# Kernel tuning notes

Hardware: AMD Instinct MI355X
Metric: run time of the kernel (lower is better)

Reference implementation:

```python
import jax, jax.numpy as jnp
import numpy as np

N_NODES = 100000
N_EDGES = 3200000
NFEAT, NHID, NCLASS = 512, 128, 40


def _glorot(key, fan_in, fan_out):
    lim = jnp.sqrt(6.0 / (fan_in + fan_out))
    return jax.random.uniform(key, (fan_in, fan_out), jnp.float32, -lim, lim)


def setup_inputs() -> dict:
    key = jax.random.key(0)
    k1, k2, k3, k4, k5 = jax.random.split(key, 5)
    x = jax.random.normal(k1, (N_NODES, NFEAT), jnp.float32)
    edge_index = jax.random.randint(k2, (2, N_EDGES), 0, N_NODES, jnp.int64)
    edge_weight = jax.random.uniform(k3, (N_EDGES,), jnp.float32)
    W1 = _glorot(k4, NFEAT, NHID)
    b1 = jnp.zeros((NHID,), jnp.float32)
    W2 = _glorot(k5, NHID, NCLASS)
    b2 = jnp.zeros((NCLASS,), jnp.float32)
    return {"x": x, "edge_index": edge_index, "edge_weight": edge_weight,
            "W1": W1, "b1": b1, "W2": W2, "b2": b2}


def _gcn_norm(edge_index, edge_weight, num_nodes):
    # add self loops (weight 1), symmetric normalization D^-1/2 A D^-1/2
    loop = jnp.arange(num_nodes, dtype=edge_index.dtype)
    row = jnp.concatenate([edge_index[0], loop])
    col = jnp.concatenate([edge_index[1], loop])
    w = jnp.concatenate([edge_weight, jnp.ones((num_nodes,), edge_weight.dtype)])
    deg = jax.ops.segment_sum(w, col, num_segments=num_nodes)
    dinv = jnp.where(deg > 0, jax.lax.rsqrt(jnp.maximum(deg, 1e-20)), 0.0)
    norm = dinv[row] * w * dinv[col]
    return row, col, norm


def _gcn_conv(h, row, col, norm, W, b, num_nodes):
    h = h @ W                                  # [N, out]
    msg = norm[:, None] * h[row]               # per-edge gather + scale
    out = jax.ops.segment_sum(msg, col, num_segments=num_nodes)  # scatter-add
    return out + b


def reference(x, edge_index, edge_weight, W1, b1, W2, b2):
    n = x.shape[0]
    row, col, norm = _gcn_norm(edge_index, edge_weight, n)
    h = jax.nn.relu(_gcn_conv(x, row, col, norm, W1, b1, n))
    # dropout: eval mode (training=False) -> identity
    return _gcn_conv(h, row, col, norm, W2, b2, n)
```

## Files before the change

kernel.cpp:

```cpp
#include <hip/hip_runtime.h>

#define NN 100000
#define NE 3200000
#define NF 512
#define NH 128
#define NC 40
#define NBIN 196
#define BINW 512
#define CAP  20480
#define EPB  4096

typedef __attribute__((ext_vector_type(8))) short bfrag;
typedef __attribute__((ext_vector_type(4))) float f32x4;
typedef __attribute__((ext_vector_type(8))) unsigned short u16x8;

static __device__ __forceinline__ unsigned short f2bf(float x) {
  unsigned u = __float_as_uint(x);
  u += 0x7FFF + ((u >> 16) & 1);
  return (unsigned short)(u >> 16);
}
static __device__ __forceinline__ float bf2f(unsigned short b) {
  return __uint_as_float(((unsigned)b) << 16);
}
static __device__ __forceinline__ float bflo(unsigned u) { return __uint_as_float(u << 16); }
static __device__ __forceinline__ float bfhi(unsigned u) { return __uint_as_float(u & 0xFFFF0000u); }


__global__ __launch_bounds__(256) void k_wconv(const float* __restrict__ W1,
                                               unsigned short* __restrict__ Wfh,
                                               unsigned short* __restrict__ Wfl,
                                               int* __restrict__ binfill) {
  if (blockIdx.x == 0 && threadIdx.x < NBIN) binfill[threadIdx.x] = 0;
  int i = blockIdx.x * 256 + threadIdx.x;
  int k = i >> 7, n = i & 127;
  float w = W1[i];
  unsigned short hi = f2bf(w);
  unsigned short lo = f2bf(w - bf2f(hi));
  int idx = ((k >> 3) * 128 + n) * 8 + (k & 7);
  Wfh[idx] = hi; Wfl[idx] = lo;
}


__global__ __launch_bounds__(256) void k_binA(const int* __restrict__ row, const int* __restrict__ col,
                                              const float* __restrict__ w,
                                              int* __restrict__ binfill, int2* __restrict__ binned) {
  __shared__ int hist[NBIN];
  __shared__ int base[NBIN];
  int t = threadIdx.x;
  int eb = blockIdx.x * EPB;
  for (int i = t; i < NBIN; i += 256) hist[i] = 0;
  __syncthreads();
  int rk[16], bn[16], sr[16]; float wv[16];
#pragma unroll
  for (int j = 0; j < 16; ++j) {
    int e = eb + t + j * 256;
    if (e < NE) {
      int c = __builtin_nontemporal_load(col + e);
      bn[j] = c >> 9;
      sr[j] = __builtin_nontemporal_load(row + e) | ((c & 511) << 17);
      wv[j] = __builtin_nontemporal_load(w + e);
      rk[j] = atomicAdd(&hist[bn[j]], 1);
    } else bn[j] = -1;
  }
  __syncthreads();
  if (t < NBIN) { int hv = hist[t]; base[t] = hv ? atomicAdd(&binfill[t], hv) : 0; }
  __syncthreads();
#pragma unroll
  for (int j = 0; j < 16; ++j) {
    if (bn[j] >= 0) {
      int pos = base[bn[j]] + rk[j];
      if (pos < CAP) binned[(size_t)bn[j] * CAP + pos] = make_int2(sr[j], __float_as_int(wv[j]));
    }
  }
}


__global__ __launch_bounds__(256) void k_binscan(const int* __restrict__ binfill,
                                                 int* __restrict__ binptr, int* __restrict__ rowptr) {
  __shared__ int sm[256];
  int t = threadIdx.x;
  sm[t] = (t < NBIN) ? binfill[t] : 0;
  __syncthreads();
  for (int off = 1; off < 256; off <<= 1) {
    int a = (t >= off) ? sm[t - off] : 0;
    __syncthreads();
    sm[t] += a;
    __syncthreads();
  }
  if (t <= NBIN) binptr[t] = (t == 0) ? 0 : sm[t - 1];
  if (t == 0) rowptr[NN] = NE;
}


__global__ __launch_bounds__(256) void k_binB(const int* __restrict__ binfill, const int* __restrict__ binptr,
                                              const int2* __restrict__ binned, int2* __restrict__ pair,
                                              int* __restrict__ rowptr, float* __restrict__ dinv) {
  __shared__ unsigned long long pk[BINW];
  __shared__ unsigned short lrank[CAP];
  __shared__ int lptr[BINW];
  __shared__ int sm[256];
  int t = threadIdx.x;
  int bin = blockIdx.x;
  int cnt = binfill[bin]; if (cnt > CAP) cnt = CAP;
  int bb = binptr[bin];
  pk[t] = 0ULL; pk[t + 256] = 0ULL;
  __syncthreads();
  const int2* src = binned + (size_t)bin * CAP;
  for (int i = t; i < cnt; i += 256) {
    int2 r = src[i];
    int lc = (unsigned)r.x >> 17;
    unsigned long long fw = (unsigned long long)(unsigned)(__int_as_float(r.y) * 16777216.0f + 0.5f);
    unsigned long long old = atomicAdd(&pk[lc], (1ULL << 42) | fw);
    lrank[i] = (unsigned short)(old >> 42);
  }
  __syncthreads();
  int c0 = (int)(pk[2 * t] >> 42), c1 = (int)(pk[2 * t + 1] >> 42);
  sm[t] = c0 + c1;
  __syncthreads();
  for (int off = 1; off < 256; off <<= 1) {
    int a = (t >= off) ? sm[t - off] : 0;
    __syncthreads();
    sm[t] += a;
    __syncthreads();
  }
  int excl = (t == 0) ? 0 : sm[t - 1];
  lptr[2 * t] = excl;
  lptr[2 * t + 1] = excl + c0;
  int n0 = bin * BINW + 2 * t;
  if (n0 < NN) {
    rowptr[n0] = bb + excl;
    float d = (float)(pk[2 * t] & 0x3FFFFFFFFFFULL) * (1.0f / 16777216.0f) + 1.0f;
    dinv[n0] = rsqrtf(d);
  }
  if (n0 + 1 < NN) {
    rowptr[n0 + 1] = bb + excl + c0;
    float d = (float)(pk[2 * t + 1] & 0x3FFFFFFFFFFULL) * (1.0f / 16777216.0f) + 1.0f;
    dinv[n0 + 1] = rsqrtf(d);
  }
  __syncthreads();
  for (int i = t; i < cnt; i += 256) {
    int2 r = src[i];
    int lc = (unsigned)r.x >> 17;
    int pos = bb + lptr[lc] + (int)lrank[i];
    pair[pos] = make_int2(r.x & 0x1FFFF, r.y);
  }
}


__global__ __launch_bounds__(256) void k_gemm1(const float* __restrict__ X,
                                               const unsigned short* __restrict__ Wfh,
                                               const unsigned short* __restrict__ Wfl,
                                               const float* __restrict__ dinv,
                                               unsigned short* __restrict__ HXb) {
  __shared__ unsigned short Ah[4096], Bh[4096], Bl[4096];
  int t = threadIdx.x;
  int lane = t & 63;
  int wid = t >> 6;
  int m0 = blockIdx.x * 128;
  int sm = t & 127;
  int skh = t >> 7;
  const float* xrow = X + (size_t)(m0 + sm) * NF + skh * 16;
  bool mok = (m0 + sm) < NN;
  int wm = wid >> 1, wn = wid & 1;
  int mb = wm * 64, nb = wn * 64;
  int fr = lane & 15, fg = lane >> 4;

  f32x4 acc[4][4];
#pragma unroll
  for (int i = 0; i < 4; ++i)
#pragma unroll
    for (int j = 0; j < 4; ++j) acc[i][j] = (f32x4)0.0f;

  for (int ks = 0; ks < 16; ++ks) {
    const u16x8* sh = (const u16x8*)(Wfh + (size_t)ks * 4096);
    const u16x8* sl = (const u16x8*)(Wfl + (size_t)ks * 4096);
    u16x8 b0 = sh[t], b1 = sh[t + 256];
    u16x8 c0 = sl[t], c1 = sl[t + 256];
    float4 xv[4];
#pragma unroll
    for (int q = 0; q < 4; ++q) {
      xv[q] = mok ? *(const float4*)(xrow + ks * 32 + q * 4)
                  : make_float4(0.f, 0.f, 0.f, 0.f);
    }
#pragma unroll
    for (int q = 0; q < 4; ++q) {
      float f[4] = {xv[q].x, xv[q].y, xv[q].z, xv[q].w};
      unsigned short h[4];
#pragma unroll
      for (int j = 0; j < 4; ++j) h[j] = f2bf(f[j]);
      int lk = skh * 16 + q * 4;
      int base = ((lk >> 3) * 128 + sm) * 8 + (lk & 7);
      uint2 hv = make_uint2((unsigned)h[0] | ((unsigned)h[1] << 16),
                            (unsigned)h[2] | ((unsigned)h[3] << 16));
      *(uint2*)&Ah[base] = hv;
    }
    ((u16x8*)Bh)[t] = b0; ((u16x8*)Bh)[t + 256] = b1;
    ((u16x8*)Bl)[t] = c0; ((u16x8*)Bl)[t + 256] = c1;
    __syncthreads();
    bfrag ah[4], bh[4], bl[4];
#pragma unroll
    for (int mi = 0; mi < 4; ++mi)
      ah[mi] = *(bfrag*)&Ah[(fg * 128 + mb + mi * 16 + fr) * 8];
#pragma unroll
    for (int nt = 0; nt < 4; ++nt) {
      int idx = (fg * 128 + nb + nt * 16 + fr) * 8;
      bh[nt] = *(bfrag*)&Bh[idx];
      bl[nt] = *(bfrag*)&Bl[idx];
    }
#pragma unroll
    for (int mi = 0; mi < 4; ++mi)
#pragma unroll
      for (int nt = 0; nt < 4; ++nt) {
        acc[mi][nt] = __builtin_amdgcn_mfma_f32_16x16x32_bf16(ah[mi], bh[nt], acc[mi][nt], 0, 0, 0);
        acc[mi][nt] = __builtin_amdgcn_mfma_f32_16x16x32_bf16(ah[mi], bl[nt], acc[mi][nt], 0, 0, 0);
      }
    __syncthreads();
  }
#pragma unroll
  for (int mi = 0; mi < 4; ++mi) {
    int rb = m0 + mb + mi * 16 + fg * 4;
#pragma unroll
    for (int q = 0; q < 4; ++q) {
      int r = rb + q;
      if (r < NN) {
        float dv = dinv[r];
#pragma unroll
        for (int nt = 0; nt < 4; ++nt) {
          int c = nb + nt * 16 + fr;
          __builtin_nontemporal_store(f2bf(dv * acc[mi][nt][q]), HXb + (size_t)r * NH + c);
        }
      }
    }
  }
}


#define FMA8(n, v)                                            \
  { unsigned uu[4] = {(v).x, (v).y, (v).z, (v).w};            \
    _Pragma("unroll")                                         \
    for (int q = 0; q < 4; ++q) {                             \
      ax[q] = fmaf((n), bflo(uu[q]), ax[q]);                  \
      ay[q] = fmaf((n), bfhi(uu[q]), ay[q]);                  \
    } }

__global__ __launch_bounds__(256) void k_agg1(const int* __restrict__ rowptr, const int2* __restrict__ pair,
                                              const unsigned* __restrict__ hxb, const float* __restrict__ dinv,
                                              const float* __restrict__ b1, unsigned* __restrict__ hb) {
  int wid = (blockIdx.x * 256 + threadIdx.x) >> 6;
  int lane = threadIdx.x & 63;
  if (wid >= NN) return;
  int sub = lane >> 4, fl = lane & 15;
  int beg = rowptr[wid], end = rowptr[wid + 1];
  const uint4* hx4 = (const uint4*)hxb;
  const long long* pr = (const long long*)pair;
  float ax[4] = {0.f, 0.f, 0.f, 0.f}, ay[4] = {0.f, 0.f, 0.f, 0.f};
  int e = beg;
  for (; e + 16 <= end; e += 16) {
    long long r0 = pr[e + sub];
    long long r1 = pr[e + 4 + sub];
    long long r2 = pr[e + 8 + sub];
    long long r3 = pr[e + 12 + sub];
    uint4 v0 = hx4[(size_t)(unsigned)(r0 & 0x1FFFF) * 16 + fl];
    uint4 v1 = hx4[(size_t)(unsigned)(r1 & 0x1FFFF) * 16 + fl];
    uint4 v2 = hx4[(size_t)(unsigned)(r2 & 0x1FFFF) * 16 + fl];
    uint4 v3 = hx4[(size_t)(unsigned)(r3 & 0x1FFFF) * 16 + fl];
    float n0 = __int_as_float((int)(r0 >> 32));
    float n1 = __int_as_float((int)(r1 >> 32));
    float n2 = __int_as_float((int)(r2 >> 32));
    float n3 = __int_as_float((int)(r3 >> 32));
    FMA8(n0, v0);
    FMA8(n1, v1);
    FMA8(n2, v2);
    FMA8(n3, v3);
  }
  for (; e + 8 <= end; e += 8) {
    long long r0 = pr[e + sub];
    long long r1 = pr[e + 4 + sub];
    uint4 v0 = hx4[(size_t)(unsigned)(r0 & 0x1FFFF) * 16 + fl];
    uint4 v1 = hx4[(size_t)(unsigned)(r1 & 0x1FFFF) * 16 + fl];
    float n0 = __int_as_float((int)(r0 >> 32));
    float n1 = __int_as_float((int)(r1 >> 32));
    FMA8(n0, v0);
    FMA8(n1, v1);
  }
  for (; e < end; e += 4) {
    int idx = e + sub;
    bool ok = idx < end;
    long long r0 = ok ? pr[idx] : 0;
    unsigned s = ok ? (unsigned)(r0 & 0x1FFFF) : (unsigned)wid;
    float n0 = ok ? __int_as_float((int)(r0 >> 32)) : 0.f;
    uint4 v0 = hx4[(size_t)s * 16 + fl];
    FMA8(n0, v0);
  }
  if (sub == 0) {
    uint4 ov = hx4[(size_t)wid * 16 + fl];
    FMA8(1.0f, ov);
  }
#pragma unroll
  for (int q = 0; q < 4; ++q) {
    ax[q] += __shfl_xor(ax[q], 16, 64); ay[q] += __shfl_xor(ay[q], 16, 64);
    ax[q] += __shfl_xor(ax[q], 32, 64); ay[q] += __shfl_xor(ay[q], 32, 64);
  }
  if (sub == 0) {
    float di = dinv[wid];
    float4 bA = ((const float4*)b1)[fl * 2];
    float4 bB = ((const float4*)b1)[fl * 2 + 1];
    float bxs[4] = {bA.x, bA.z, bB.x, bB.z};
    float bys[4] = {bA.y, bA.w, bB.y, bB.w};
    unsigned o[4];
#pragma unroll
    for (int q = 0; q < 4; ++q) {
      float rx = fmaxf(fmaf(di, ax[q], bxs[q]), 0.f);
      float ry = fmaxf(fmaf(di, ay[q], bys[q]), 0.f);
      o[q] = (unsigned)f2bf(rx) | ((unsigned)f2bf(ry) << 16);
    }
    ((uint4*)hb)[(size_t)wid * 16 + fl] = make_uint4(o[0], o[1], o[2], o[3]);
  }
}


__global__ __launch_bounds__(256) void k_gemm2(const unsigned* __restrict__ hb, const float* __restrict__ W2,
                                               const float* __restrict__ dinv,
                                               unsigned short* __restrict__ H2b) {
  __shared__ float Hs[32][132];
  __shared__ float Ws[NH * NC];
  int t = threadIdx.x;
  int m0 = blockIdx.x * 32;
  {
    int r = t >> 3, cb = (t & 7) * 8;
    int rowi = m0 + r;
    if (rowi < NN) {
      uint4 a = *(const uint4*)(hb + (size_t)rowi * 64 + cb);
      uint4 b = *(const uint4*)(hb + (size_t)rowi * 64 + cb + 4);
      unsigned u[8] = {a.x, a.y, a.z, a.w, b.x, b.y, b.z, b.w};
#pragma unroll
      for (int j = 0; j < 8; ++j) {
        Hs[r][cb * 2 + j * 2]     = bflo(u[j]);
        Hs[r][cb * 2 + j * 2 + 1] = bfhi(u[j]);
      }
    } else {
#pragma unroll
      for (int j = 0; j < 16; ++j) Hs[r][cb * 2 + j] = 0.f;
    }
  }
  for (int i = t; i < NH * NC; i += 256) Ws[i] = W2[i];
  __syncthreads();
  int r = t >> 3, c0 = (t & 7) * 5;
  float acc[5] = {0.f, 0.f, 0.f, 0.f, 0.f};
#pragma unroll 4
  for (int k = 0; k < NH; ++k) {
    float hv = Hs[r][k];
#pragma unroll
    for (int j = 0; j < 5; ++j) acc[j] = fmaf(hv, Ws[k * NC + c0 + j], acc[j]);
  }
  int rowi = m0 + r;
  if (rowi < NN) {
    float dv = dinv[rowi];
#pragma unroll
    for (int j = 0; j < 5; ++j)
      __builtin_nontemporal_store(f2bf(dv * acc[j]), H2b + (size_t)rowi * 64 + c0 + j);
    int prr = t & 7;
    if (prr < 3) {
#pragma unroll
      for (int j = 0; j < 8; ++j)
        __builtin_nontemporal_store((unsigned short)0, H2b + (size_t)rowi * 64 + 40 + prr * 8 + j);
    }
  }
}


#define FMA4(n, v)                                            \
  { unsigned uu[2] = {(v).x, (v).y};                          \
    _Pragma("unroll")                                         \
    for (int q = 0; q < 2; ++q) {                             \
      ax[q] = fmaf((n), bflo(uu[q]), ax[q]);                  \
      ay[q] = fmaf((n), bfhi(uu[q]), ay[q]);                  \
    } }

__global__ __launch_bounds__(256) void k_agg2(const int* __restrict__ rowptr, const int2* __restrict__ pair,
                                              const unsigned* __restrict__ h2u,
                                              const float* __restrict__ dinv,
                                              const float* __restrict__ b2, float* __restrict__ out) {
  int wid = (blockIdx.x * 256 + threadIdx.x) >> 6;
  int lane = threadIdx.x & 63;
  if (wid >= NN) return;
  int sub = lane >> 4, fl = lane & 15;
  int beg = rowptr[wid], end = rowptr[wid + 1];
  const uint2* h4 = (const uint2*)h2u;
  const long long* pr = (const long long*)pair;
  float ax[2] = {0.f, 0.f}, ay[2] = {0.f, 0.f};
  int e = beg;
  for (; e + 16 <= end; e += 16) {
    long long r0 = pr[e + sub];
    long long r1 = pr[e + 4 + sub];
    long long r2 = pr[e + 8 + sub];
    long long r3 = pr[e + 12 + sub];
    uint2 v0 = h4[(size_t)(unsigned)(r0 & 0x1FFFF) * 16 + fl];
    uint2 v1 = h4[(size_t)(unsigned)(r1 & 0x1FFFF) * 16 + fl];
    uint2 v2 = h4[(size_t)(unsigned)(r2 & 0x1FFFF) * 16 + fl];
    uint2 v3 = h4[(size_t)(unsigned)(r3 & 0x1FFFF) * 16 + fl];
    float n0 = __int_as_float((int)(r0 >> 32));
    float n1 = __int_as_float((int)(r1 >> 32));
    float n2 = __int_as_float((int)(r2 >> 32));
    float n3 = __int_as_float((int)(r3 >> 32));
    FMA4(n0, v0);
    FMA4(n1, v1);
    FMA4(n2, v2);
    FMA4(n3, v3);
  }
  for (; e + 8 <= end; e += 8) {
    long long r0 = pr[e + sub];
    long long r1 = pr[e + 4 + sub];
    uint2 v0 = h4[(size_t)(unsigned)(r0 & 0x1FFFF) * 16 + fl];
    uint2 v1 = h4[(size_t)(unsigned)(r1 & 0x1FFFF) * 16 + fl];
    float n0 = __int_as_float((int)(r0 >> 32));
    float n1 = __int_as_float((int)(r1 >> 32));
    FMA4(n0, v0);
    FMA4(n1, v1);
  }
  for (; e < end; e += 4) {
    int idx = e + sub;
    bool ok = idx < end;
    long long r0 = ok ? pr[idx] : 0;
    unsigned s = ok ? (unsigned)(r0 & 0x1FFFF) : (unsigned)wid;
    float n0 = ok ? __int_as_float((int)(r0 >> 32)) : 0.f;
    uint2 v0 = h4[(size_t)s * 16 + fl];
    FMA4(n0, v0);
  }
  if (sub == 0) {
    uint2 ov = h4[(size_t)wid * 16 + fl];
    FMA4(1.0f, ov);
  }
#pragma unroll
  for (int q = 0; q < 2; ++q) {
    ax[q] += __shfl_xor(ax[q], 16, 64); ay[q] += __shfl_xor(ay[q], 16, 64);
    ax[q] += __shfl_xor(ax[q], 32, 64); ay[q] += __shfl_xor(ay[q], 32, 64);
  }
  if (sub == 0 && fl < 10) {
    float di = dinv[wid];
    float4 bv = ((const float4*)b2)[fl];
    float4 o = make_float4(fmaf(di, ax[0], bv.x), fmaf(di, ay[0], bv.y),
                           fmaf(di, ax[1], bv.z), fmaf(di, ay[1], bv.w));
    *(float4*)(out + (size_t)wid * NC + fl * 4) = o;
  }
}


extern "C" void kernel_launch(void* const* d_in, const int* in_sizes, int n_in,
                              void* d_out, int out_size, void* d_ws, size_t ws_size,
                              hipStream_t stream) {
  const float* x  = (const float*)d_in[0];
  const int*   ei = (const int*)d_in[1];
  const float* ew = (const float*)d_in[2];
  const float* W1 = (const float*)d_in[3];
  const float* b1 = (const float*)d_in[4];
  const float* W2 = (const float*)d_in[5];
  const float* b2 = (const float*)d_in[6];
  float* out = (float*)d_out;
  const int* row = ei;
  const int* col = ei + NE;

  char* ws = (char*)d_ws;
  size_t o = 0;
  auto alloc = [&](size_t bytes) -> void* {
    void* p = ws + o;
    o += (bytes + 255) & ~(size_t)255;
    return p;
  };
  float* dinv    = (float*)alloc((size_t)NN * 4);
  int*   rowptr  = (int*)alloc((size_t)(NN + 1) * 4);
  int*   binfill = (int*)alloc(1024);
  int*   binptr  = (int*)alloc(1024);
  int2*  pair    = (int2*)alloc((size_t)NE * 8);
  unsigned short* Wfh = (unsigned short*)alloc((size_t)NF * NH * 2);
  unsigned short* Wfl = (unsigned short*)alloc((size_t)NF * NH * 2);
  unsigned short* hxb = (unsigned short*)alloc((size_t)NN * NH * 2);
  unsigned*       hb  = (unsigned*)alloc((size_t)NN * NH * 2);
  int2*  binned  = (int2*)alloc((size_t)NBIN * CAP * 8);
  unsigned short* h2b = (unsigned short*)hxb;

  k_wconv<<<(NF * NH) / 256, 256, 0, stream>>>(W1, Wfh, Wfl, binfill);
  k_binA<<<(NE + EPB - 1) / EPB, 256, 0, stream>>>(row, col, ew, binfill, binned);
  k_binscan<<<1, 256, 0, stream>>>(binfill, binptr, rowptr);
  k_binB<<<NBIN, 256, 0, stream>>>(binfill, binptr, binned, pair, rowptr, dinv);
  k_gemm1<<<(NN + 127) / 128, 256, 0, stream>>>(x, Wfh, Wfl, dinv, hxb);
  k_agg1<<<(NN * 64) / 256, 256, 0, stream>>>(rowptr, pair, (const unsigned*)hxb, dinv, b1, hb);
  k_gemm2<<<(NN + 31) / 32, 256, 0, stream>>>(hb, W2, dinv, h2b);
  k_agg2<<<(NN * 64) / 256, 256, 0, stream>>>(rowptr, pair, (const unsigned*)h2b, dinv, b2, out);
}
```

Baseline: 400.8 us.

## Double-buffer LDS and prefetch next K-slice in first GEMM

```diff
diff --git a/kernel.cpp b/kernel.cpp
--- a/kernel.cpp
+++ b/kernel.cpp
@@ -152,7 +152,7 @@
                                                const unsigned short* __restrict__ Wfl,
                                                const float* __restrict__ dinv,
                                                unsigned short* __restrict__ HXb) {
-  __shared__ unsigned short Ah[4096], Bh[4096], Bl[4096];
+  __shared__ unsigned short Ah[2][4096], Bh[2][4096], Bl[2][4096];
   int t = threadIdx.x;
   int lane = t & 63;
   int wid = t >> 6;
@@ -171,17 +171,20 @@
 #pragma unroll
     for (int j = 0; j < 4; ++j) acc[i][j] = (f32x4)0.0f;
 
+  u16x8 vb0, vb1, vc0, vc1;
+  float4 xv[4];
+  {
+    const u16x8* sh = (const u16x8*)Wfh;
+    const u16x8* sl = (const u16x8*)Wfl;
+    vb0 = sh[t]; vb1 = sh[t + 256];
+    vc0 = sl[t]; vc1 = sl[t + 256];
+#pragma unroll
+    for (int q = 0; q < 4; ++q)
+      xv[q] = mok ? *(const float4*)(xrow + q * 4) : make_float4(0.f, 0.f, 0.f, 0.f);
+  }
+
   for (int ks = 0; ks < 16; ++ks) {
-    const u16x8* sh = (const u16x8*)(Wfh + (size_t)ks * 4096);
-    const u16x8* sl = (const u16x8*)(Wfl + (size_t)ks * 4096);
-    u16x8 b0 = sh[t], b1 = sh[t + 256];
-    u16x8 c0 = sl[t], c1 = sl[t + 256];
-    float4 xv[4];
-#pragma unroll
-    for (int q = 0; q < 4; ++q) {
-      xv[q] = mok ? *(const float4*)(xrow + ks * 32 + q * 4)
-                  : make_float4(0.f, 0.f, 0.f, 0.f);
-    }
+    int cur = ks & 1;
 #pragma unroll
     for (int q = 0; q < 4; ++q) {
       float f[4] = {xv[q].x, xv[q].y, xv[q].z, xv[q].w};
@@ -192,20 +195,30 @@
       int base = ((lk >> 3) * 128 + sm) * 8 + (lk & 7);
       uint2 hv = make_uint2((unsigned)h[0] | ((unsigned)h[1] << 16),
                             (unsigned)h[2] | ((unsigned)h[3] << 16));
-      *(uint2*)&Ah[base] = hv;
-    }
-    ((u16x8*)Bh)[t] = b0; ((u16x8*)Bh)[t + 256] = b1;
-    ((u16x8*)Bl)[t] = c0; ((u16x8*)Bl)[t + 256] = c1;
+      *(uint2*)&Ah[cur][base] = hv;
+    }
+    ((u16x8*)Bh[cur])[t] = vb0; ((u16x8*)Bh[cur])[t + 256] = vb1;
+    ((u16x8*)Bl[cur])[t] = vc0; ((u16x8*)Bl[cur])[t + 256] = vc1;
+    if (ks < 15) {
+      const u16x8* sh = (const u16x8*)(Wfh + (size_t)(ks + 1) * 4096);
+      const u16x8* sl = (const u16x8*)(Wfl + (size_t)(ks + 1) * 4096);
+      vb0 = sh[t]; vb1 = sh[t + 256];
+      vc0 = sl[t]; vc1 = sl[t + 256];
+#pragma unroll
+      for (int q = 0; q < 4; ++q)
+        xv[q] = mok ? *(const float4*)(xrow + (ks + 1) * 32 + q * 4)
+                    : make_float4(0.f, 0.f, 0.f, 0.f);
+    }
     __syncthreads();
     bfrag ah[4], bh[4], bl[4];
 #pragma unroll
     for (int mi = 0; mi < 4; ++mi)
-      ah[mi] = *(bfrag*)&Ah[(fg * 128 + mb + mi * 16 + fr) * 8];
+      ah[mi] = *(bfrag*)&Ah[cur][(fg * 128 + mb + mi * 16 + fr) * 8];
 #pragma unroll
     for (int nt = 0; nt < 4; ++nt) {
       int idx = (fg * 128 + nb + nt * 16 + fr) * 8;
-      bh[nt] = *(bfrag*)&Bh[idx];
-      bl[nt] = *(bfrag*)&Bl[idx];
+      bh[nt] = *(bfrag*)&Bh[cur][idx];
+      bl[nt] = *(bfrag*)&Bl[cur][idx];
     }
 #pragma unroll
     for (int mi = 0; mi < 4; ++mi)
@@ -214,7 +227,6 @@
         acc[mi][nt] = __builtin_amdgcn_mfma_f32_16x16x32_bf16(ah[mi], bh[nt], acc[mi][nt], 0, 0, 0);
         acc[mi][nt] = __builtin_amdgcn_mfma_f32_16x16x32_bf16(ah[mi], bl[nt], acc[mi][nt], 0, 0, 0);
       }
-    __syncthreads();
   }
 #pragma unroll
   for (int mi = 0; mi < 4; ++mi) {
```

Measured after the change: 392.6 us. 1.02x faster.
